# Optimization experiments

Hardware: AMD Instinct MI355X
Metric: run time of the kernel (lower is better)

Reference implementation:

```python
import jax, jax.numpy as jnp
import numpy as np

D = 1024      # input_dim
H = 4096      # hidden_dim
E = 8         # expert_count
TOP_K = 2
N = 8192      # tokens
LN_EPS = 1e-5


def setup_inputs() -> dict:
    key = jax.random.key(0)
    ks = jax.random.split(key, 10)
    s_d = 1.0 / np.sqrt(D)
    s_h = 1.0 / np.sqrt(H)
    return {
        "x": jax.random.normal(ks[0], (N, D), dtype=jnp.float32),
        "ln_gamma": jnp.ones((D,), jnp.float32),
        "ln_beta": jnp.zeros((D,), jnp.float32),
        "conf_w": jax.random.uniform(ks[1], (D, 1), jnp.float32, -s_d, s_d),
        "conf_b": jnp.zeros((1,), jnp.float32),
        "router_w": jax.random.uniform(ks[2], (D, E), jnp.float32, -s_d, s_d),
        "router_b": jnp.zeros((E,), jnp.float32),
        "w1": jax.random.uniform(ks[3], (E, D, H), jnp.float32, -s_d, s_d),
        "b1": jax.random.uniform(ks[4], (E, H), jnp.float32, -s_d, s_d),
        "w2": jax.random.uniform(ks[5], (E, H, D), jnp.float32, -s_h, s_h),
        "b2": jax.random.uniform(ks[6], (E, D), jnp.float32, -s_h, s_h),
    }


def reference(x, ln_gamma, ln_beta, conf_w, conf_b, router_w, router_b, w1, b1, w2, b2):
    # LayerNorm (torch default eps=1e-5, affine)
    mu = jnp.mean(x, axis=-1, keepdims=True)
    var = jnp.mean(jnp.square(x - mu), axis=-1, keepdims=True)
    x_norm = (x - mu) * jax.lax.rsqrt(var + LN_EPS) * ln_gamma + ln_beta

    # layer-skip confidence head
    confidence = jax.nn.sigmoid(x_norm @ conf_w + conf_b)  # [N,1]

    # router: softmax -> top-k -> renormalize selected weights
    router_probs = jax.nn.softmax(x_norm @ router_w + router_b, axis=-1)  # [N,E]
    vals, indices = jax.lax.top_k(router_probs, TOP_K)                    # [N,K]
    vals = vals / jnp.sum(vals, axis=-1, keepdims=True)

    # scatter top-k weights into dense per-expert combine weights [N,E]
    combine_w = jnp.zeros((x.shape[0], E), x.dtype).at[
        jnp.arange(x.shape[0])[:, None], indices].add(vals)

    # dispatch/combine: loop over small fixed expert count (dense compute,
    # weighted by combine_w, mathematically identical to per-token dispatch)
    combined = jnp.zeros_like(x)
    for e in range(E):
        h = jax.nn.relu(x_norm @ w1[e] + b1[e])      # [N,H]
        combined = combined + combine_w[:, e:e + 1] * (h @ w2[e] + b2[e])

    output = x + combined
    return output, confidence, x
```

## Files before the change

kernel.cpp:

```cpp
#include <hip/hip_runtime.h>
#include <hip/hip_bf16.h>

#define N_TOK 8192
#define DIM   1024
#define HID   4096
#define NEXP  8
#define CSTR  64
#define RTMAX 136
#define HROWS 16896
#define EPS   264

using bf16x8 = __attribute__((ext_vector_type(8))) short;
using f32x4  = __attribute__((ext_vector_type(4))) float;

__device__ __forceinline__ void gload_lds16(const void* g, void* l) {
  __builtin_amdgcn_global_load_lds(
      (const __attribute__((address_space(1))) unsigned int*)g,
      (__attribute__((address_space(3))) unsigned int*)l, 16, 0, 0);
}

__device__ __forceinline__ float wredsum(float v) {
#pragma unroll
  for (int off = 32; off > 0; off >>= 1) v += __shfl_xor(v, off, 64);
  return v;
}

__device__ __forceinline__ unsigned short f2bf(float f) {
  __hip_bfloat16 h = __float2bfloat16(f);
  return *reinterpret_cast<unsigned short*>(&h);
}
__device__ __forceinline__ float bf2f(unsigned short u) {
  return __uint_as_float((unsigned)u << 16);
}

__device__ __forceinline__ void transpose_body(
    const float* __restrict__ src, __hip_bfloat16* __restrict__ dst,
    int R, int C, int c0, int r0, float (*tile)[65]) {
  const int tid = threadIdx.x;
  const int tx = tid & 15, ty = tid >> 4;
#pragma unroll
  for (int k = 0; k < 4; k++) {
    const int row = ty + k * 16;
    const float4 v = *(const float4*)(src + (size_t)(r0 + row) * C + c0 + tx * 4);
    tile[row][tx * 4 + 0] = v.x; tile[row][tx * 4 + 1] = v.y;
    tile[row][tx * 4 + 2] = v.z; tile[row][tx * 4 + 3] = v.w;
  }
  __syncthreads();
#pragma unroll
  for (int k = 0; k < 4; k++) {
    const int orow = ty + k * 16;
    ushort4 st;
    st.x = f2bf(tile[tx * 4 + 0][orow]);
    st.y = f2bf(tile[tx * 4 + 1][orow]);
    st.z = f2bf(tile[tx * 4 + 2][orow]);
    st.w = f2bf(tile[tx * 4 + 3][orow]);
    *(ushort4*)((unsigned short*)dst + (size_t)(c0 + orow) * R + r0 + tx * 4) = st;
  }
}

__global__ __launch_bounds__(256) void setup_kernel(
    const float* __restrict__ x, const float* __restrict__ gamma, const float* __restrict__ beta,
    const float* __restrict__ conf_w, const float* __restrict__ conf_b,
    const float* __restrict__ rw, const float* __restrict__ rb,
    const float* __restrict__ w1, const float* __restrict__ w2,
    __hip_bfloat16* __restrict__ w1t, __hip_bfloat16* __restrict__ w2t,
    __hip_bfloat16* __restrict__ xn, float* __restrict__ out,
    int* __restrict__ counts, int* __restrict__ lists, float* __restrict__ wts,
    int2* __restrict__ idx) {
  __shared__ float tile[64][65];
  const int b = (int)blockIdx.x;
  if (b < 8192) {
    const int z = b >> 10, r = b & 1023;
    const int cx = r & 63, ry = r >> 6;
    transpose_body(w1 + (size_t)z * DIM * HID, w1t + (size_t)z * DIM * HID,
                   DIM, HID, cx * 64, ry * 64, tile);
    return;
  }
  if (b < 16384) {
    const int bb = b - 8192;
    const int z = bb >> 10, r = bb & 1023;
    const int cx = r & 15, ry = r >> 4;
    transpose_body(w2 + (size_t)z * HID * DIM, w2t + (size_t)z * HID * DIM,
                   HID, DIM, cx * 64, ry * 64, tile);
    return;
  }
  const int t = (b - 16384) * 4 + ((int)threadIdx.x >> 6);
  const int lane = threadIdx.x & 63;
  const float* xr = x + (size_t)t * DIM;

  float4 xv[4];
#pragma unroll
  for (int q = 0; q < 4; q++) xv[q] = *(const float4*)(xr + q * 256 + lane * 4);

  float s = 0.f, s2 = 0.f;
#pragma unroll
  for (int q = 0; q < 4; q++) {
    s  += xv[q].x + xv[q].y + xv[q].z + xv[q].w;
    s2 += xv[q].x * xv[q].x + xv[q].y * xv[q].y + xv[q].z * xv[q].z + xv[q].w * xv[q].w;
  }
  s = wredsum(s); s2 = wredsum(s2);
  const float mu  = s * (1.f / DIM);
  const float inv = rsqrtf(s2 * (1.f / DIM) - mu * mu + 1e-5f);

  float p[9];
#pragma unroll
  for (int e = 0; e < 9; e++) p[e] = 0.f;

#pragma unroll
  for (int q = 0; q < 4; q++) {
    const int d0 = q * 256 + lane * 4;
    const float4 g4 = *(const float4*)(gamma + d0);
    const float4 b4 = *(const float4*)(beta + d0);
    float v0 = (xv[q].x - mu) * inv * g4.x + b4.x;
    float v1 = (xv[q].y - mu) * inv * g4.y + b4.y;
    float v2 = (xv[q].z - mu) * inv * g4.z + b4.z;
    float v3 = (xv[q].w - mu) * inv * g4.w + b4.w;

    ushort4 st; st.x = f2bf(v0); st.y = f2bf(v1); st.z = f2bf(v2); st.w = f2bf(v3);
    *(ushort4*)((unsigned short*)xn + (size_t)t * DIM + d0) = st;
    *(float4*)(out + (size_t)t * DIM + d0) = xv[q];
    *(float4*)(out + (size_t)N_TOK * DIM + N_TOK + (size_t)t * DIM + d0) = xv[q];

    const float vv[4] = {v0, v1, v2, v3};
#pragma unroll
    for (int j = 0; j < 4; j++) {
      const int d = d0 + j;
      const float v = vv[j];
      p[8] += v * conf_w[d];
      const float4 r0 = *(const float4*)(rw + d * 8);
      const float4 r1 = *(const float4*)(rw + d * 8 + 4);
      p[0] += v * r0.x; p[1] += v * r0.y; p[2] += v * r0.z; p[3] += v * r0.w;
      p[4] += v * r1.x; p[5] += v * r1.y; p[6] += v * r1.z; p[7] += v * r1.w;
    }
  }
#pragma unroll
  for (int e = 0; e < 9; e++) p[e] = wredsum(p[e]);

  if (lane == 0) {
    float L[8];
#pragma unroll
    for (int e = 0; e < 8; e++) L[e] = p[e] + rb[e];
    const float cl = p[8] + conf_b[0];
    out[(size_t)N_TOK * DIM + t] = 1.f / (1.f + expf(-cl));

    float mx = L[0];
#pragma unroll
    for (int e = 1; e < 8; e++) mx = fmaxf(mx, L[e]);
    float pe[8];
#pragma unroll
    for (int e = 0; e < 8; e++) pe[e] = expf(L[e] - mx);
    int i0 = 0; float v0 = pe[0];
#pragma unroll
    for (int e = 1; e < 8; e++) if (pe[e] > v0) { v0 = pe[e]; i0 = e; }
    int i1 = -1; float v1 = -1.f;
#pragma unroll
    for (int e = 0; e < 8; e++) if (e != i0 && pe[e] > v1) { v1 = pe[e]; i1 = e; }
    const float wsum = v0 + v1;
    const float w0 = v0 / wsum, w1v = v1 / wsum;
    int p0 = atomicAdd(&counts[i0 * CSTR], 1);
    lists[i0 * N_TOK + p0] = t; wts[i0 * N_TOK + p0] = w0;
    int p1 = atomicAdd(&counts[i1 * CSTR], 1);
    lists[i1 * N_TOK + p1] = t; wts[i1 * N_TOK + p1] = w1v;
    idx[t] = make_int2((i0 << 13) | p0, (i1 << 13) | p1);
  }
}

__global__ void bases_kernel(const int* __restrict__ counts, int* __restrict__ bases,
                             int* __restrict__ meta) {
  if (threadIdx.x == 0) {
    int s = 0, r = 0;
#pragma unroll
    for (int e = 0; e < NEXP; e++) {
      bases[e] = s; meta[e] = r;
      const int c = counts[e * CSTR];
      s += c; r += (c + 127) >> 7;
    }
    meta[NEXP] = r;
  }
}


#define LGKM_SB(N)                                                            \
  asm volatile("s_waitcnt lgkmcnt(" #N ")" ::: "memory");                     \
  __builtin_amdgcn_sched_barrier(0);

#define MFMA_G(MI)                                                            \
  __builtin_amdgcn_s_setprio(1);                                              \
  _Pragma("unroll")                                                           \
  for (int n = 0; n < 4; n++)                                                 \
    acc[MI][n] = __builtin_amdgcn_mfma_f32_16x16x32_bf16(afr[MI], bfr[n], acc[MI][n], 0, 0, 0); \
  __builtin_amdgcn_s_setprio(0);

#define GEMM_CORE(NT)                                                                   \
  f32x4 acc[8][4] = {};                                                                 \
  stage(0, 0); stage(1, 24576);                                                         \
  for (int t = 0; t < (NT); ++t) {                                                      \
    const int pb = (t % 3) * 24576;                                                     \
    if (t + 1 < (NT)) { asm volatile("s_waitcnt vmcnt(6)" ::: "memory"); }              \
    else              { asm volatile("s_waitcnt vmcnt(0)" ::: "memory"); }              \
    __builtin_amdgcn_s_barrier();                                                       \
    if (t + 2 < (NT)) stage(t + 2, ((t + 2) % 3) * 24576);                              \
    const char* Ab = smem + pb + Abase;                                                 \
    const char* Bb = smem + pb + Bbase;                                                 \
    bf16x8 bfr[4], afr[8];                                                              \
    afr[0] = *(const bf16x8*)(Ab);                                                      \
    bfr[0] = *(const bf16x8*)(Bb);                                                      \
    bfr[1] = *(const bf16x8*)(Bb + 1024);                                               \
    __builtin_amdgcn_sched_barrier(0);                                                  \
    bfr[2] = *(const bf16x8*)(Bb + 2048);                                               \
    bfr[3] = *(const bf16x8*)(Bb + 3072);                                               \
    __builtin_amdgcn_sched_barrier(0);                                                  \
    _Pragma("unroll")                                                                   \
    for (int m = 1; m < 8; m++) {                                                       \
      afr[m] = *(const bf16x8*)(Ab + m * 1024);                                         \
      __builtin_amdgcn_sched_barrier(0);                                                \
    }                                                                                   \
    LGKM_SB(7) MFMA_G(0)                                                                \
    LGKM_SB(6) MFMA_G(1)                                                                \
    LGKM_SB(5) MFMA_G(2)                                                                \
    LGKM_SB(4) MFMA_G(3)                                                                \
    LGKM_SB(3) MFMA_G(4)                                                                \
    LGKM_SB(2) MFMA_G(5)                                                                \
    LGKM_SB(1) MFMA_G(6)                                                                \
    LGKM_SB(0) MFMA_G(7)                                                                \
  }

#define DECODE_TAIL()                                                         \
  if (rtg >= meta[NEXP]) return;                                              \
  int e = 0;                                                                  \
  _Pragma("unroll")                                                           \
  for (int k = 1; k < NEXP; k++) if (meta[k] <= rtg) e = k;                   \
  const int rt = rtg - meta[e];                                               \
  const int cnt = counts[e * CSTR];                                           \
  const int hbase = bases[e];

#define GEMM_COMMON()                                                         \
  __shared__ char smem[73728];                                                \
  const int tid = threadIdx.x;                     \
  const int l = tid & 63;                                                     \
  const int wc = tid >> 6;                                                    \
  const int lr = l & 15;                                                      \
  const int pchunk = (l >> 4) ^ ((lr >> 1) & 3);                              \
  const int Abase = lr * 64 + pchunk * 16;                                    \
  const int Bbase = 8192 + (wc * 64 + lr) * 64 + pchunk * 16;                 \
  const int srow = tid >> 2;                       \
  const int lc = (tid & 3) ^ ((srow >> 1) & 3);

#define EPILOGUE(DSTROW)                                                      \
  __builtin_amdgcn_s_barrier();                                               \
  {                                                                           \
    unsigned short* ep = (unsigned short*)smem;                               \
    _Pragma("unroll")                                                         \
    for (int n = 0; n < 4; n++) {                                             \
      const int col = wc * 64 + n * 16 + lr;                                  \
      _Pragma("unroll")                                                       \
      for (int m = 0; m < 8; m++) {                                           \
        f32x4 v = acc[m][n];                                                  \
        _Pragma("unroll")                                                     \
        for (int j = 0; j < 4; j++) {                                         \
          const int row = m * 16 + (l >> 4) * 4 + j;                          \
          ep[row * EPS + col] = f2bf(v[j]);                                   \
        }                                                                     \
      }                                                                       \
    }                                                                         \
    asm volatile("s_waitcnt lgkmcnt(0)" ::: "memory");                        \
    __builtin_amdgcn_s_barrier();                                             \
    const int g = tid >> 5, u = tid & 31;                                     \
    _Pragma("unroll")                                                         \
    for (int i = 0; i < 16; i++) {                                            \
      const int row = i * 8 + g;                                              \
      const int pos = rt * 128 + row;                                         \
      if (pos < cnt) {                                                        \
        bf16x8 vv = *(const bf16x8*)(ep + row * EPS + u * 8);                 \
        *(bf16x8*)(DSTROW + u * 8) = vv;                                      \
      }                                                                       \
    }                                                                         \
  }

__global__ __launch_bounds__(256, 2) void gemm1_kernel(
    const __hip_bfloat16* __restrict__ xn, const __hip_bfloat16* __restrict__ w1t_b,
    const float* __restrict__ b1, const int* __restrict__ lists,
    const int* __restrict__ counts, const int* __restrict__ bases,
    const int* __restrict__ meta, __hip_bfloat16* __restrict__ hbuf) {
  const int x_ = (int)blockIdx.x & 7;
  const int q_ = (int)blockIdx.x >> 3;
  const int rtg = q_ >> 1;
  const int panel = x_ * 2 + (q_ & 1);
  DECODE_TAIL()
  const int ct = panel;
  const int* list = lists + e * N_TOK;
  const __hip_bfloat16* w1t = w1t_b + (size_t)e * DIM * HID;
  GEMM_COMMON()

  const int ap0 = rt * 128 + srow, ap1 = ap0 + 64;
  const int tok0 = list[ap0 < cnt ? ap0 : 0];
  const int tok1 = list[ap1 < cnt ? ap1 : 0];
  const unsigned short* srcA0 = (const unsigned short*)xn + (size_t)tok0 * DIM + lc * 8;
  const unsigned short* srcA1 = (const unsigned short*)xn + (size_t)tok1 * DIM + lc * 8;
  const unsigned short* srcB0 = (const unsigned short*)w1t + (size_t)(ct * 256 + srow) * DIM + lc * 8;
  const unsigned short* srcB1 = (const unsigned short*)w1t + (size_t)(ct * 256 + 64 + srow) * DIM + lc * 8;
  const unsigned short* srcB2 = (const unsigned short*)w1t + (size_t)(ct * 256 + 128 + srow) * DIM + lc * 8;
  const unsigned short* srcB3 = (const unsigned short*)w1t + (size_t)(ct * 256 + 192 + srow) * DIM + lc * 8;

  auto stage = [&](int tt, int lbase) {
    gload_lds16(srcA0 + tt * 32, smem + lbase + tid * 16);
    gload_lds16(srcA1 + tt * 32, smem + lbase + 4096 + tid * 16);
    gload_lds16(srcB0 + tt * 32, smem + lbase + 8192 + tid * 16);
    gload_lds16(srcB1 + tt * 32, smem + lbase + 12288 + tid * 16);
    gload_lds16(srcB2 + tt * 32, smem + lbase + 16384 + tid * 16);
    gload_lds16(srcB3 + tt * 32, smem + lbase + 20480 + tid * 16);
  };

  GEMM_CORE(DIM / 32)

  const float bv[4] = {
    b1[e * HID + ct * 256 + wc * 64 + 0 * 16 + lr],
    b1[e * HID + ct * 256 + wc * 64 + 1 * 16 + lr],
    b1[e * HID + ct * 256 + wc * 64 + 2 * 16 + lr],
    b1[e * HID + ct * 256 + wc * 64 + 3 * 16 + lr]};
#pragma unroll
  for (int n = 0; n < 4; n++)
#pragma unroll
    for (int m = 0; m < 8; m++)
#pragma unroll
      for (int j = 0; j < 4; j++) acc[m][n][j] = fmaxf(acc[m][n][j] + bv[n], 0.f);
  EPILOGUE((unsigned short*)hbuf + (size_t)(hbase + pos) * HID + ct * 256)
}

__global__ __launch_bounds__(256, 2) void gemm2_kernel(
    const __hip_bfloat16* __restrict__ hbuf, const __hip_bfloat16* __restrict__ w2t_b,
    const int* __restrict__ counts, const int* __restrict__ bases,
    const int* __restrict__ meta, __hip_bfloat16* __restrict__ ybuf, const int SK) {
  int panel, rtg;
  if (SK == 2) {
    const int x_ = (int)blockIdx.x & 7;
    const int q_ = (int)blockIdx.x >> 3;
    rtg = (q_ >> 2) * 4 + (x_ >> 1);
    panel = (x_ & 1) * 4 + (q_ & 3);
  } else {
    panel = (int)blockIdx.x / RTMAX;
    rtg = (int)blockIdx.x - panel * RTMAX;
  }
  DECODE_TAIL()
  const int ct = panel & 3;
  const int ksp = panel >> 2;
  const int kbase = ksp * (HID / SK);
  const __hip_bfloat16* w2t = w2t_b + (size_t)e * DIM * HID;
  GEMM_COMMON()

  const unsigned short* srcA0 = (const unsigned short*)hbuf +
      (size_t)(hbase + rt * 128 + srow) * HID + kbase + lc * 8;
  const unsigned short* srcA1 = (const unsigned short*)hbuf +
      (size_t)(hbase + rt * 128 + 64 + srow) * HID + kbase + lc * 8;
  const unsigned short* srcB0 = (const unsigned short*)w2t +
      (size_t)(ct * 256 + srow) * HID + kbase + lc * 8;
  const unsigned short* srcB1 = (const unsigned short*)w2t +
      (size_t)(ct * 256 + 64 + srow) * HID + kbase + lc * 8;
  const unsigned short* srcB2 = (const unsigned short*)w2t +
      (size_t)(ct * 256 + 128 + srow) * HID + kbase + lc * 8;
  const unsigned short* srcB3 = (const unsigned short*)w2t +
      (size_t)(ct * 256 + 192 + srow) * HID + kbase + lc * 8;

  auto stage = [&](int tt, int lbase) {
    gload_lds16(srcA0 + tt * 32, smem + lbase + tid * 16);
    gload_lds16(srcA1 + tt * 32, smem + lbase + 4096 + tid * 16);
    gload_lds16(srcB0 + tt * 32, smem + lbase + 8192 + tid * 16);
    gload_lds16(srcB1 + tt * 32, smem + lbase + 12288 + tid * 16);
    gload_lds16(srcB2 + tt * 32, smem + lbase + 16384 + tid * 16);
    gload_lds16(srcB3 + tt * 32, smem + lbase + 20480 + tid * 16);
  };

  const int nk = (HID / 32) / SK;
  GEMM_CORE(nk)

  EPILOGUE((unsigned short*)ybuf + ((size_t)ksp * HROWS + hbase + pos) * DIM + ct * 256)
}

__global__ __launch_bounds__(256) void combine_kernel(
    const __hip_bfloat16* __restrict__ ybuf, const float* __restrict__ b2,
    const int2* __restrict__ idx, const float* __restrict__ wv,
    const int* __restrict__ bases, float* __restrict__ out, const int SK) {
  const int t = blockIdx.x * 4 + (threadIdx.x >> 6);
  const int lane = threadIdx.x & 63;
  const int2 iv = idx[t];
  const int e0 = iv.x >> 13, p0 = iv.x & (N_TOK - 1);
  const int e1 = iv.y >> 13, p1 = iv.y & (N_TOK - 1);
  const float w0 = wv[iv.x], w1 = wv[iv.y];
  const int r0 = bases[e0] + p0;
  const int r1 = bases[e1] + p1;
#pragma unroll
  for (int q = 0; q < 4; q++) {
    const int d0 = q * 256 + lane * 4;
    float4 o = *(const float4*)(out + (size_t)t * DIM + d0);
    float y0x = 0.f, y0y = 0.f, y0z = 0.f, y0w = 0.f;
    float y1x = 0.f, y1y = 0.f, y1z = 0.f, y1w = 0.f;
    for (int s = 0; s < SK; s++) {
      const ushort4 a = *(const ushort4*)((const unsigned short*)ybuf +
                          ((size_t)s * HROWS + r0) * DIM + d0);
      const ushort4 b = *(const ushort4*)((const unsigned short*)ybuf +
                          ((size_t)s * HROWS + r1) * DIM + d0);
      y0x += bf2f(a.x); y0y += bf2f(a.y); y0z += bf2f(a.z); y0w += bf2f(a.w);
      y1x += bf2f(b.x); y1y += bf2f(b.y); y1z += bf2f(b.z); y1w += bf2f(b.w);
    }
    const float4 bb0 = *(const float4*)(b2 + e0 * DIM + d0);
    const float4 bb1 = *(const float4*)(b2 + e1 * DIM + d0);
    o.x += w0 * (y0x + bb0.x) + w1 * (y1x + bb1.x);
    o.y += w0 * (y0y + bb0.y) + w1 * (y1y + bb1.y);
    o.z += w0 * (y0z + bb0.z) + w1 * (y1z + bb1.z);
    o.w += w0 * (y0w + bb0.w) + w1 * (y1w + bb1.w);
    *(float4*)(out + (size_t)t * DIM + d0) = o;
  }
}

extern "C" void kernel_launch(void* const* d_in, const int* in_sizes, int n_in,
                              void* d_out, int out_size, void* d_ws, size_t ws_size,
                              hipStream_t stream) {
  (void)in_sizes; (void)n_in; (void)out_size;
  const float* x      = (const float*)d_in[0];
  const float* gamma  = (const float*)d_in[1];
  const float* beta   = (const float*)d_in[2];
  const float* conf_w = (const float*)d_in[3];
  const float* conf_b = (const float*)d_in[4];
  const float* rw     = (const float*)d_in[5];
  const float* rb     = (const float*)d_in[6];
  const float* w1     = (const float*)d_in[7];
  const float* b1     = (const float*)d_in[8];
  const float* w2     = (const float*)d_in[9];
  const float* b2     = (const float*)d_in[10];
  float* out = (float*)d_out;

  char* w = (char*)d_ws;
  auto alloc = [&](size_t bytes) { char* p = w; w += (bytes + 255) & ~255ULL; return p; };

  __hip_bfloat16* xn = (__hip_bfloat16*)alloc((size_t)N_TOK * DIM * 2);
  int*   lists  = (int*)alloc((size_t)NEXP * N_TOK * 4);
  float* wtsb   = (float*)alloc((size_t)NEXP * N_TOK * 4);
  int*   counts = (int*)alloc(NEXP * CSTR * 4);
  int*   bases  = (int*)alloc(256);
  int*   meta   = (int*)alloc(256);
  int2*  idx    = (int2*)alloc((size_t)N_TOK * 8);

  const size_t hbufA = (size_t)HROWS * HID * 2;
  const size_t wtA   = (size_t)NEXP * DIM * HID * 2;
  __hip_bfloat16* hbuf = (__hip_bfloat16*)alloc(hbufA);
  __hip_bfloat16* w1t  = (__hip_bfloat16*)alloc(wtA);
  __hip_bfloat16* w2t  = (__hip_bfloat16*)alloc(wtA);
  const size_t used = (size_t)(w - (char*)d_ws);
  const size_t ybuf1 = (size_t)HROWS * DIM * 2;

  int SK;
  __hip_bfloat16* ybuf;
  if (ws_size >= used + 2 * ybuf1 + 4096) {
    SK = 2; ybuf = (__hip_bfloat16*)alloc(2 * ybuf1);
  } else {
    SK = 1; ybuf = w1t;
  }
  const int g2grid = (SK == 2) ? 8 * RTMAX : 4 * RTMAX;

  hipMemsetAsync(counts, 0, NEXP * CSTR * 4, stream);
  setup_kernel<<<16384 + N_TOK / 4, 256, 0, stream>>>(
      x, gamma, beta, conf_w, conf_b, rw, rb, w1, w2, w1t, w2t,
      xn, out, counts, lists, wtsb, idx);
  bases_kernel<<<1, 64, 0, stream>>>(counts, bases, meta);
  gemm1_kernel<<<8 * 2 * RTMAX, 256, 0, stream>>>(xn, w1t, b1, lists, counts, bases, meta,
                                                  hbuf);
  gemm2_kernel<<<g2grid, 256, 0, stream>>>(hbuf, w2t, counts, bases, meta, ybuf, SK);
  combine_kernel<<<N_TOK / 4, 256, 0, stream>>>(ybuf, b2, idx, wtsb, bases, out, SK);
}
```

Measured before the change: 487.0 us.

## Grow expert GEMM tiles to 256x256 with 512-thread blocks, drop redundant x copy

Both expert GEMMs move from 128x256 tiles on 256 threads to 256x256 tiles on 512 threads (8 waves laid out 2x4). This uses more LDS per stage and a two-pass epilogue, and row-tile granularity becomes 256 tokens. The intent is to halve weight-tile reloads per output and raise arithmetic intensity. The cost is more padding waste per expert and lower occupancy. Separately, setup no longer writes x into out, and combine reads the residual straight from x, which removes one full write and read of the output.

```diff
diff --git a/kernel.cpp b/kernel.cpp
--- a/kernel.cpp
+++ b/kernel.cpp
@@ -6,7 +6,7 @@
 #define HID   4096
 #define NEXP  8
 #define CSTR  64
-#define RTMAX 136
+#define RTMAX 72
 #define HROWS 16896
 #define EPS   264
 
@@ -118,7 +118,6 @@
 
     ushort4 st; st.x = f2bf(v0); st.y = f2bf(v1); st.z = f2bf(v2); st.w = f2bf(v3);
     *(ushort4*)((unsigned short*)xn + (size_t)t * DIM + d0) = st;
-    *(float4*)(out + (size_t)t * DIM + d0) = xv[q];
     *(float4*)(out + (size_t)N_TOK * DIM + N_TOK + (size_t)t * DIM + d0) = xv[q];
 
     const float vv[4] = {v0, v1, v2, v3};
@@ -173,7 +172,7 @@
     for (int e = 0; e < NEXP; e++) {
       bases[e] = s; meta[e] = r;
       const int c = counts[e * CSTR];
-      s += c; r += (c + 127) >> 7;
+      s += c; r += (c + 255) >> 8;
     }
     meta[NEXP] = r;
   }
@@ -193,13 +192,13 @@
 
 #define GEMM_CORE(NT)                                                                   \
   f32x4 acc[8][4] = {};                                                                 \
-  stage(0, 0); stage(1, 24576);                                                         \
+  stage(0, 0); stage(1, 32768);                                                         \
   for (int t = 0; t < (NT); ++t) {                                                      \
-    const int pb = (t % 3) * 24576;                                                     \
-    if (t + 1 < (NT)) { asm volatile("s_waitcnt vmcnt(6)" ::: "memory"); }              \
+    const int pb = (t % 3) * 32768;                                                     \
+    if (t + 1 < (NT)) { asm volatile("s_waitcnt vmcnt(4)" ::: "memory"); }              \
     else              { asm volatile("s_waitcnt vmcnt(0)" ::: "memory"); }              \
     __builtin_amdgcn_s_barrier();                                                       \
-    if (t + 2 < (NT)) stage(t + 2, ((t + 2) % 3) * 24576);                              \
+    if (t + 2 < (NT)) stage(t + 2, ((t + 2) % 3) * 32768);                              \
     const char* Ab = smem + pb + Abase;                                                 \
     const char* Bb = smem + pb + Bbase;                                                 \
     bf16x8 bfr[4], afr[8];                                                              \
@@ -235,15 +234,17 @@
   const int hbase = bases[e];
 
 #define GEMM_COMMON()                                                         \
-  __shared__ char smem[73728];                                                \
+  __shared__ char smem[98304];                                                \
   const int tid = threadIdx.x;                     \
   const int l = tid & 63;                                                     \
-  const int wc = tid >> 6;                                                    \
+  const int w8 = tid >> 6;                                                    \
+  const int wr = w8 >> 2;                                                     \
+  const int wc = w8 & 3;                                                      \
   const int lr = l & 15;                                                      \
   const int pchunk = (l >> 4) ^ ((lr >> 1) & 3);                              \
-  const int Abase = lr * 64 + pchunk * 16;                                    \
-  const int Bbase = 8192 + (wc * 64 + lr) * 64 + pchunk * 16;                 \
-  const int srow = tid >> 2;                       \
+  const int Abase = (wr * 128 + lr) * 64 + pchunk * 16;                       \
+  const int Bbase = 16384 + (wc * 64 + lr) * 64 + pchunk * 16;                \
+  const int srow = tid >> 2;                      \
   const int lc = (tid & 3) ^ ((srow >> 1) & 3);
 
 #define EPILOGUE(DSTROW)                                                      \
@@ -251,33 +252,37 @@
   {                                                                           \
     unsigned short* ep = (unsigned short*)smem;                               \
     _Pragma("unroll")                                                         \
-    for (int n = 0; n < 4; n++) {                                             \
-      const int col = wc * 64 + n * 16 + lr;                                  \
-      _Pragma("unroll")                                                       \
-      for (int m = 0; m < 8; m++) {                                           \
-        f32x4 v = acc[m][n];                                                  \
+    for (int h = 0; h < 2; h++) {                                             \
+      if (wr == h) {                                                          \
         _Pragma("unroll")                                                     \
-        for (int j = 0; j < 4; j++) {                                         \
-          const int row = m * 16 + (l >> 4) * 4 + j;                          \
-          ep[row * EPS + col] = f2bf(v[j]);                                   \
+        for (int n = 0; n < 4; n++) {                                         \
+          const int col = wc * 64 + n * 16 + lr;                              \
+          _Pragma("unroll")                                                   \
+          for (int m = 0; m < 8; m++) {                                       \
+            f32x4 v = acc[m][n];                                              \
+            _Pragma("unroll")                                                 \
+            for (int j = 0; j < 4; j++)                                       \
+              ep[(m * 16 + (l >> 4) * 4 + j) * EPS + col] = f2bf(v[j]);       \
+          }                                                                   \
         }                                                                     \
       }                                                                       \
+      asm volatile("s_waitcnt lgkmcnt(0)" ::: "memory");                      \
+      __builtin_amdgcn_s_barrier();                                           \
+      const int g = tid >> 5, u = tid & 31;                                   \
+      _Pragma("unroll")                                                       \
+      for (int i = 0; i < 8; i++) {                                           \
+        const int row = i * 16 + g;                                           \
+        const int pos = rt * 256 + h * 128 + row;                             \
+        if (pos < cnt) {                                                      \
+          bf16x8 vv = *(const bf16x8*)(ep + row * EPS + u * 8);               \
+          *(bf16x8*)(DSTROW + u * 8) = vv;                                    \
+        }                                                                     \
+      }                                                                       \
+      __builtin_amdgcn_s_barrier();                                           \
     }                                                                         \
-    asm volatile("s_waitcnt lgkmcnt(0)" ::: "memory");                        \
-    __builtin_amdgcn_s_barrier();                                             \
-    const int g = tid >> 5, u = tid & 31;                                     \
-    _Pragma("unroll")                                                         \
-    for (int i = 0; i < 16; i++) {                                            \
-      const int row = i * 8 + g;                                              \
-      const int pos = rt * 128 + row;                                         \
-      if (pos < cnt) {                                                        \
-        bf16x8 vv = *(const bf16x8*)(ep + row * EPS + u * 8);                 \
-        *(bf16x8*)(DSTROW + u * 8) = vv;                                      \
-      }                                                                       \
-    }                                                                         \
-  }
-
-__global__ __launch_bounds__(256, 2) void gemm1_kernel(
+  }
+
+__global__ __launch_bounds__(512, 2) void gemm1_kernel(
     const __hip_bfloat16* __restrict__ xn, const __hip_bfloat16* __restrict__ w1t_b,
     const float* __restrict__ b1, const int* __restrict__ lists,
     const int* __restrict__ counts, const int* __restrict__ bases,
@@ -292,23 +297,19 @@
   const __hip_bfloat16* w1t = w1t_b + (size_t)e * DIM * HID;
   GEMM_COMMON()
 
-  const int ap0 = rt * 128 + srow, ap1 = ap0 + 64;
+  const int ap0 = rt * 256 + srow, ap1 = ap0 + 128;
   const int tok0 = list[ap0 < cnt ? ap0 : 0];
   const int tok1 = list[ap1 < cnt ? ap1 : 0];
   const unsigned short* srcA0 = (const unsigned short*)xn + (size_t)tok0 * DIM + lc * 8;
   const unsigned short* srcA1 = (const unsigned short*)xn + (size_t)tok1 * DIM + lc * 8;
   const unsigned short* srcB0 = (const unsigned short*)w1t + (size_t)(ct * 256 + srow) * DIM + lc * 8;
-  const unsigned short* srcB1 = (const unsigned short*)w1t + (size_t)(ct * 256 + 64 + srow) * DIM + lc * 8;
-  const unsigned short* srcB2 = (const unsigned short*)w1t + (size_t)(ct * 256 + 128 + srow) * DIM + lc * 8;
-  const unsigned short* srcB3 = (const unsigned short*)w1t + (size_t)(ct * 256 + 192 + srow) * DIM + lc * 8;
+  const unsigned short* srcB1 = (const unsigned short*)w1t + (size_t)(ct * 256 + 128 + srow) * DIM + lc * 8;
 
   auto stage = [&](int tt, int lbase) {
     gload_lds16(srcA0 + tt * 32, smem + lbase + tid * 16);
-    gload_lds16(srcA1 + tt * 32, smem + lbase + 4096 + tid * 16);
-    gload_lds16(srcB0 + tt * 32, smem + lbase + 8192 + tid * 16);
-    gload_lds16(srcB1 + tt * 32, smem + lbase + 12288 + tid * 16);
-    gload_lds16(srcB2 + tt * 32, smem + lbase + 16384 + tid * 16);
-    gload_lds16(srcB3 + tt * 32, smem + lbase + 20480 + tid * 16);
+    gload_lds16(srcA1 + tt * 32, smem + lbase + 8192 + tid * 16);
+    gload_lds16(srcB0 + tt * 32, smem + lbase + 16384 + tid * 16);
+    gload_lds16(srcB1 + tt * 32, smem + lbase + 24576 + tid * 16);
   };
 
   GEMM_CORE(DIM / 32)
@@ -327,7 +328,7 @@
   EPILOGUE((unsigned short*)hbuf + (size_t)(hbase + pos) * HID + ct * 256)
 }
 
-__global__ __launch_bounds__(256, 2) void gemm2_kernel(
+__global__ __launch_bounds__(512, 2) void gemm2_kernel(
     const __hip_bfloat16* __restrict__ hbuf, const __hip_bfloat16* __restrict__ w2t_b,
     const int* __restrict__ counts, const int* __restrict__ bases,
     const int* __restrict__ meta, __hip_bfloat16* __restrict__ ybuf, const int SK) {
@@ -349,25 +350,19 @@
   GEMM_COMMON()
 
   const unsigned short* srcA0 = (const unsigned short*)hbuf +
-      (size_t)(hbase + rt * 128 + srow) * HID + kbase + lc * 8;
+      (size_t)(hbase + rt * 256 + srow) * HID + kbase + lc * 8;
   const unsigned short* srcA1 = (const unsigned short*)hbuf +
-      (size_t)(hbase + rt * 128 + 64 + srow) * HID + kbase + lc * 8;
+      (size_t)(hbase + rt * 256 + 128 + srow) * HID + kbase + lc * 8;
   const unsigned short* srcB0 = (const unsigned short*)w2t +
       (size_t)(ct * 256 + srow) * HID + kbase + lc * 8;
   const unsigned short* srcB1 = (const unsigned short*)w2t +
-      (size_t)(ct * 256 + 64 + srow) * HID + kbase + lc * 8;
-  const unsigned short* srcB2 = (const unsigned short*)w2t +
       (size_t)(ct * 256 + 128 + srow) * HID + kbase + lc * 8;
-  const unsigned short* srcB3 = (const unsigned short*)w2t +
-      (size_t)(ct * 256 + 192 + srow) * HID + kbase + lc * 8;
 
   auto stage = [&](int tt, int lbase) {
     gload_lds16(srcA0 + tt * 32, smem + lbase + tid * 16);
-    gload_lds16(srcA1 + tt * 32, smem + lbase + 4096 + tid * 16);
-    gload_lds16(srcB0 + tt * 32, smem + lbase + 8192 + tid * 16);
-    gload_lds16(srcB1 + tt * 32, smem + lbase + 12288 + tid * 16);
-    gload_lds16(srcB2 + tt * 32, smem + lbase + 16384 + tid * 16);
-    gload_lds16(srcB3 + tt * 32, smem + lbase + 20480 + tid * 16);
+    gload_lds16(srcA1 + tt * 32, smem + lbase + 8192 + tid * 16);
+    gload_lds16(srcB0 + tt * 32, smem + lbase + 16384 + tid * 16);
+    gload_lds16(srcB1 + tt * 32, smem + lbase + 24576 + tid * 16);
   };
 
   const int nk = (HID / 32) / SK;
@@ -377,9 +372,10 @@
 }
 
 __global__ __launch_bounds__(256) void combine_kernel(
-    const __hip_bfloat16* __restrict__ ybuf, const float* __restrict__ b2,
-    const int2* __restrict__ idx, const float* __restrict__ wv,
-    const int* __restrict__ bases, float* __restrict__ out, const int SK) {
+    const float* __restrict__ x, const __hip_bfloat16* __restrict__ ybuf,
+    const float* __restrict__ b2, const int2* __restrict__ idx,
+    const float* __restrict__ wv, const int* __restrict__ bases,
+    float* __restrict__ out, const int SK) {
   const int t = blockIdx.x * 4 + (threadIdx.x >> 6);
   const int lane = threadIdx.x & 63;
   const int2 iv = idx[t];
@@ -391,7 +387,7 @@
 #pragma unroll
   for (int q = 0; q < 4; q++) {
     const int d0 = q * 256 + lane * 4;
-    float4 o = *(const float4*)(out + (size_t)t * DIM + d0);
+    float4 o = *(const float4*)(x + (size_t)t * DIM + d0);
     float y0x = 0.f, y0y = 0.f, y0z = 0.f, y0w = 0.f;
     float y1x = 0.f, y1y = 0.f, y1z = 0.f, y1w = 0.f;
     for (int s = 0; s < SK; s++) {
@@ -462,8 +458,8 @@
       x, gamma, beta, conf_w, conf_b, rw, rb, w1, w2, w1t, w2t,
       xn, out, counts, lists, wtsb, idx);
   bases_kernel<<<1, 64, 0, stream>>>(counts, bases, meta);
-  gemm1_kernel<<<8 * 2 * RTMAX, 256, 0, stream>>>(xn, w1t, b1, lists, counts, bases, meta,
+  gemm1_kernel<<<8 * 2 * RTMAX, 512, 0, stream>>>(xn, w1t, b1, lists, counts, bases, meta,
                                                   hbuf);
-  gemm2_kernel<<<g2grid, 256, 0, stream>>>(hbuf, w2t, counts, bases, meta, ybuf, SK);
-  combine_kernel<<<N_TOK / 4, 256, 0, stream>>>(ybuf, b2, idx, wtsb, bases, out, SK);
-}
+  gemm2_kernel<<<g2grid, 512, 0, stream>>>(hbuf, w2t, counts, bases, meta, ybuf, SK);
+  combine_kernel<<<N_TOK / 4, 256, 0, stream>>>(x, ybuf, b2, idx, wtsb, bases, out, SK);
+}
```

Measured after the change: 509.1 us. 1.05x slower.

## Move w2 transpose into gemm1 launch and read residual from x directly

Applied to the files above, without the earlier changes.

The w2 fp32-to-bf16 transpose blocks move from the setup kernel into extra blocks appended to the gemm1 grid. The transpose then overlaps with the first expert GEMM instead of sitting on the critical path before routing and gemm1. The setup kernel also stops copying x into the output, and combine reads the residual from x directly, removing one full-size write. The risk is that the heavy transpose blocks share shared memory and CUs with the gemm1 blocks, and the launch order may leave them running as a tail.

```diff
diff --git a/kernel.cpp b/kernel.cpp
--- a/kernel.cpp
+++ b/kernel.cpp
@@ -9,6 +9,7 @@
 #define RTMAX 136
 #define HROWS 16896
 #define EPS   264
+#define NG1   (8 * 2 * RTMAX)
 
 using bf16x8 = __attribute__((ext_vector_type(8))) short;
 using f32x4  = __attribute__((ext_vector_type(4))) float;
@@ -62,8 +63,8 @@
     const float* __restrict__ x, const float* __restrict__ gamma, const float* __restrict__ beta,
     const float* __restrict__ conf_w, const float* __restrict__ conf_b,
     const float* __restrict__ rw, const float* __restrict__ rb,
-    const float* __restrict__ w1, const float* __restrict__ w2,
-    __hip_bfloat16* __restrict__ w1t, __hip_bfloat16* __restrict__ w2t,
+    const float* __restrict__ w1,
+    __hip_bfloat16* __restrict__ w1t,
     __hip_bfloat16* __restrict__ xn, float* __restrict__ out,
     int* __restrict__ counts, int* __restrict__ lists, float* __restrict__ wts,
     int2* __restrict__ idx) {
@@ -76,15 +77,7 @@
                    DIM, HID, cx * 64, ry * 64, tile);
     return;
   }
-  if (b < 16384) {
-    const int bb = b - 8192;
-    const int z = bb >> 10, r = bb & 1023;
-    const int cx = r & 15, ry = r >> 4;
-    transpose_body(w2 + (size_t)z * HID * DIM, w2t + (size_t)z * HID * DIM,
-                   HID, DIM, cx * 64, ry * 64, tile);
-    return;
-  }
-  const int t = (b - 16384) * 4 + ((int)threadIdx.x >> 6);
+  const int t = (b - 8192) * 4 + ((int)threadIdx.x >> 6);
   const int lane = threadIdx.x & 63;
   const float* xr = x + (size_t)t * DIM;
 
@@ -118,7 +111,6 @@
 
     ushort4 st; st.x = f2bf(v0); st.y = f2bf(v1); st.z = f2bf(v2); st.w = f2bf(v3);
     *(ushort4*)((unsigned short*)xn + (size_t)t * DIM + d0) = st;
-    *(float4*)(out + (size_t)t * DIM + d0) = xv[q];
     *(float4*)(out + (size_t)N_TOK * DIM + N_TOK + (size_t)t * DIM + d0) = xv[q];
 
     const float vv[4] = {v0, v1, v2, v3};
@@ -235,7 +227,6 @@
   const int hbase = bases[e];
 
 #define GEMM_COMMON()                                                         \
-  __shared__ char smem[73728];                                                \
   const int tid = threadIdx.x;                     \
   const int l = tid & 63;                                                     \
   const int wc = tid >> 6;                                                    \
@@ -281,7 +272,17 @@
     const __hip_bfloat16* __restrict__ xn, const __hip_bfloat16* __restrict__ w1t_b,
     const float* __restrict__ b1, const int* __restrict__ lists,
     const int* __restrict__ counts, const int* __restrict__ bases,
-    const int* __restrict__ meta, __hip_bfloat16* __restrict__ hbuf) {
+    const int* __restrict__ meta, __hip_bfloat16* __restrict__ hbuf,
+    const float* __restrict__ w2, __hip_bfloat16* __restrict__ w2t) {
+  __shared__ char smem[73728];
+  if ((int)blockIdx.x >= NG1) {
+    const int bb = (int)blockIdx.x - NG1;
+    const int z = bb >> 10, r = bb & 1023;
+    const int cx = r & 15, ry = r >> 4;
+    transpose_body(w2 + (size_t)z * HID * DIM, w2t + (size_t)z * HID * DIM,
+                   HID, DIM, cx * 64, ry * 64, (float(*)[65])smem);
+    return;
+  }
   const int x_ = (int)blockIdx.x & 7;
   const int q_ = (int)blockIdx.x >> 3;
   const int rtg = q_ >> 1;
@@ -331,6 +332,7 @@
     const __hip_bfloat16* __restrict__ hbuf, const __hip_bfloat16* __restrict__ w2t_b,
     const int* __restrict__ counts, const int* __restrict__ bases,
     const int* __restrict__ meta, __hip_bfloat16* __restrict__ ybuf, const int SK) {
+  __shared__ char smem[73728];
   int panel, rtg;
   if (SK == 2) {
     const int x_ = (int)blockIdx.x & 7;
@@ -377,9 +379,10 @@
 }
 
 __global__ __launch_bounds__(256) void combine_kernel(
-    const __hip_bfloat16* __restrict__ ybuf, const float* __restrict__ b2,
-    const int2* __restrict__ idx, const float* __restrict__ wv,
-    const int* __restrict__ bases, float* __restrict__ out, const int SK) {
+    const float* __restrict__ x, const __hip_bfloat16* __restrict__ ybuf,
+    const float* __restrict__ b2, const int2* __restrict__ idx,
+    const float* __restrict__ wv, const int* __restrict__ bases,
+    float* __restrict__ out, const int SK) {
   const int t = blockIdx.x * 4 + (threadIdx.x >> 6);
   const int lane = threadIdx.x & 63;
   const int2 iv = idx[t];
@@ -391,7 +394,7 @@
 #pragma unroll
   for (int q = 0; q < 4; q++) {
     const int d0 = q * 256 + lane * 4;
-    float4 o = *(const float4*)(out + (size_t)t * DIM + d0);
+    float4 o = *(const float4*)(x + (size_t)t * DIM + d0);
     float y0x = 0.f, y0y = 0.f, y0z = 0.f, y0w = 0.f;
     float y1x = 0.f, y1y = 0.f, y1z = 0.f, y1w = 0.f;
     for (int s = 0; s < SK; s++) {
@@ -458,12 +461,12 @@
   const int g2grid = (SK == 2) ? 8 * RTMAX : 4 * RTMAX;
 
   hipMemsetAsync(counts, 0, NEXP * CSTR * 4, stream);
-  setup_kernel<<<16384 + N_TOK / 4, 256, 0, stream>>>(
-      x, gamma, beta, conf_w, conf_b, rw, rb, w1, w2, w1t, w2t,
+  setup_kernel<<<8192 + N_TOK / 4, 256, 0, stream>>>(
+      x, gamma, beta, conf_w, conf_b, rw, rb, w1, w1t,
       xn, out, counts, lists, wtsb, idx);
   bases_kernel<<<1, 64, 0, stream>>>(counts, bases, meta);
-  gemm1_kernel<<<8 * 2 * RTMAX, 256, 0, stream>>>(xn, w1t, b1, lists, counts, bases, meta,
-                                                  hbuf);
+  gemm1_kernel<<<NG1 + 8192, 256, 0, stream>>>(xn, w1t, b1, lists, counts, bases, meta,
+                                               hbuf, w2, w2t);
   gemm2_kernel<<<g2grid, 256, 0, stream>>>(hbuf, w2t, counts, bases, meta, ybuf, SK);
-  combine_kernel<<<N_TOK / 4, 256, 0, stream>>>(ybuf, b2, idx, wtsb, bases, out, SK);
-}
+  combine_kernel<<<N_TOK / 4, 256, 0, stream>>>(x, ybuf, b2, idx, wtsb, bases, out, SK);
+}
```

Result: faster. 459.4 us (-5.7%).
